# Performance work log

Hardware: AMD Instinct MI355X
Metric: run time of the kernel (lower is better)

The kernel has to match this reference:

```python
import jax, jax.numpy as jnp
import numpy as np

D = 33        # n_vertices
HID = 256     # hidden_features
N_RANKS = 5


def setup_inputs() -> dict:
    key = jax.random.key(0)
    ks = jax.random.split(key, 8)
    img = jax.random.uniform(ks[0], (1, 3, 2160, 3840), dtype=jnp.float32)
    param = jax.random.normal(ks[1], (1, N_RANKS), dtype=jnp.float32) * 0.1

    def lin(k, fan_in, fan_out):
        lim = 1.0 / np.sqrt(fan_in)
        kw, kb = jax.random.split(k)
        W = jax.random.uniform(kw, (fan_in, fan_out), minval=-lim, maxval=lim, dtype=jnp.float32)
        b = jax.random.uniform(kb, (fan_out,), minval=-lim, maxval=lim, dtype=jnp.float32)
        return W, b

    W0, b0 = lin(ks[2], 11, HID)
    W1, b1 = lin(ks[3], HID, HID)
    W2, b2 = lin(ks[4], HID, HID)
    W3, b3 = lin(ks[5], HID, HID)
    W4, b4 = lin(ks[6], HID, 3)
    return dict(img=img, param=param, W0=W0, b0=b0, W1=W1, b1=b1,
                W2=W2, b2=b2, W3=W3, b3=b3, W4=W4, b4=b4)


def _identity_lut_flat():
    # torch: stack(meshgrid(ij), 0)/ (D-1), flip(0), reshape (1,3,D^3)
    v = jnp.arange(D, dtype=jnp.float32)
    g = jnp.stack(jnp.meshgrid(v, v, v, indexing='ij'), axis=0) / (D - 1)
    return g[::-1].reshape(1, 3, -1)  # (1, 3, 35937)


def _nilut(intensity, W0, b0, W1, b1, W2, b2, W3, b3, W4, b4):
    # intensity: (B, N, 8) = [r, g, b, params...]
    inp = jnp.concatenate([intensity, jnp.sort(intensity[..., :3], axis=-1)], axis=-1)  # (B,N,11)
    zero_inp = inp[:1].at[:, :, 3:-3].set(0.0)  # zero the param channels

    def net(x):
        h = jax.nn.relu(x @ W0 + b0)
        h = jnp.tanh(h @ W1 + b1)
        h = jnp.tanh(h @ W2 + b2)
        h = jnp.tanh(h @ W3 + b3)
        return h @ W4 + b4

    return net(inp) - net(zero_inp) + intensity[..., :3]


def _trilinear_lookup(img, luts):
    # img: (B,3,H,W) in [0,1]; luts: (B,3,D,D,D) indexed [c, b_idx, g_idx, r_idx]
    s = img * (D - 1)
    idx = jnp.clip(jnp.floor(s), 0, D - 2).astype(jnp.int32)
    f = s - idx.astype(s.dtype)

    def one(lut_b, idx_b, f_b):
        ir, ig, ib = idx_b[0], idx_b[1], idx_b[2]
        fr, fg, fb = f_b[0], f_b[1], f_b[2]

        def g(db, dg, dr):
            return lut_b[:, ib + db, ig + dg, ir + dr]  # (3,H,W)

        return (g(0, 0, 0) * (1 - fb) * (1 - fg) * (1 - fr)
                + g(0, 0, 1) * (1 - fb) * (1 - fg) * fr
                + g(0, 1, 0) * (1 - fb) * fg * (1 - fr)
                + g(0, 1, 1) * (1 - fb) * fg * fr
                + g(1, 0, 0) * fb * (1 - fg) * (1 - fr)
                + g(1, 0, 1) * fb * (1 - fg) * fr
                + g(1, 1, 0) * fb * fg * (1 - fr)
                + g(1, 1, 1) * fb * fg * fr)

    return jax.vmap(one)(luts, idx, f)


def reference(img, param, W0, b0, W1, b1, W2, b2, W3, b3, W4, b4):
    B = param.shape[0]
    ident = _identity_lut_flat()                              # (1,3,N)
    Nl = ident.shape[2]
    tiled = jnp.broadcast_to(param[:, :, None], (B, N_RANKS, Nl))
    ins = jnp.concatenate([jnp.broadcast_to(ident, (B, 3, Nl)), tiled], axis=1)  # (B,8,N)
    ins = jnp.transpose(ins, (0, 2, 1))                       # (B,N,8)
    luts = _nilut(ins, W0, b0, W1, b1, W2, b2, W3, b3, W4, b4)  # (B,N,3)
    luts = jnp.transpose(luts, (0, 2, 1)).reshape(B, 3, D, D, D)
    img_rep = jnp.broadcast_to(img, (B,) + img.shape[1:])
    return _trilinear_lookup(img_rep, luts)
```

## Files before the change

kernel.cpp:

```cpp
#include <hip/hip_runtime.h>
#include <hip/hip_fp16.h>
#include <math.h>

#define NPTS 35937
#define HID 256
#define TPB 256

typedef __attribute__((ext_vector_type(8))) short short8;
typedef __attribute__((ext_vector_type(4))) float f32x4;

__device__ __forceinline__ float fast_tanh(float x) {
    float e = __expf(2.0f * x);
    return 1.0f - __fdividef(2.0f, e + 1.0f);
}

__device__ __forceinline__ short f2bf(float f) {
    union { float f; unsigned u; } v; v.f = f;
    unsigned r = (v.u + 0x7fffu + ((v.u >> 16) & 1u)) >> 16;
    return (short)r;
}

#define W1P_OFF 8192
#define W2P_OFF 73728
#define W3P_OFF 139264
#define W4P_OFF 204800
#define LUT_BYTE_OFF 417792
#define CELL_BYTE_OFF 992896

__global__ __launch_bounds__(256) void pack_weights_kernel(
    const float* __restrict__ W0, const float* __restrict__ W1,
    const float* __restrict__ W2, const float* __restrict__ W3,
    const float* __restrict__ W4, short* __restrict__ P)
{
    int id = blockIdx.x * 256 + threadIdx.x;
    if (id >= 26112) return;
    const float* W; int f, NT, KREAL, NROW; long pbase;
    if (id < 1024)       { W = W0; f = id;         NT = 16; KREAL = 11;  NROW = 256; pbase = 0; }
    else if (id < 9216)  { W = W1; f = id - 1024;  NT = 16; KREAL = 256; NROW = 256; pbase = W1P_OFF; }
    else if (id < 17408) { W = W2; f = id - 9216;  NT = 16; KREAL = 256; NROW = 256; pbase = W2P_OFF; }
    else if (id < 25600) { W = W3; f = id - 17408; NT = 16; KREAL = 256; NROW = 256; pbase = W3P_OFF; }
    else                 { W = W4; f = id - 25600; NT = 1;  KREAL = 256; NROW = 3;   pbase = W4P_OFF; }
    int lane = f & 63;
    int tile = f >> 6;
    int nt = tile % NT, kt = tile / NT;
    int n  = nt * 16 + (lane & 15);
    int k0 = kt * 32 + ((lane >> 4) & 3) * 8;
    short v[8];
    #pragma unroll
    for (int j = 0; j < 8; ++j) {
        int k = k0 + j;
        float x = (k < KREAL && n < NROW) ? W[k * NROW + n] : 0.0f;
        v[j] = f2bf(x);
    }
    *(short8*)(P + pbase + (long)f * 8) = *(short8*)v;
}

#define HSTR 264

__global__ __launch_bounds__(256) void nilut_mfma_kernel(
    const float* __restrict__ param, const short* __restrict__ P,
    const float* __restrict__ b0, const float* __restrict__ b1,
    const float* __restrict__ b2, const float* __restrict__ b3,
    const float* __restrict__ b4, float* __restrict__ lut4)
{
    __shared__ short Hs[64][HSTR];
    __shared__ short Is[64][40];
    __shared__ float OB[64][4];

    const int t = threadIdx.x;
    const int pblock = blockIdx.x * 32;
    const int lane = t & 63;
    const int wid  = t >> 6;
    const int lr = lane & 15;
    const int hi = lane >> 4;
    const int k8 = hi * 8;

    if (t < 64) {
        int pn = pblock + (t >> 1);
        if (pn >= NPTS) pn = NPTS - 1;
        int v = t & 1;
        int ii = pn / 1089;
        int rem = pn - ii * 1089;
        int jj = rem / 33;
        int kk = rem - jj * 33;
        float r = kk * (1.0f / 32.0f);
        float g = jj * (1.0f / 32.0f);
        float b = ii * (1.0f / 32.0f);
        float lo = fminf(r, fminf(g, b));
        float hv = fmaxf(r, fmaxf(g, b));
        float mid = r + g + b - lo - hv;
        Is[t][0] = f2bf(r); Is[t][1] = f2bf(g); Is[t][2] = f2bf(b);
        #pragma unroll
        for (int q = 0; q < 5; ++q)
            Is[t][3 + q] = (v == 0) ? f2bf(param[q]) : (short)0;
        Is[t][8] = f2bf(lo); Is[t][9] = f2bf(mid); Is[t][10] = f2bf(hv);
        #pragma unroll
        for (int q = 11; q < 40; ++q) Is[t][q] = (short)0;
    }
    __syncthreads();

    f32x4 acc[4][4];

    {
        #pragma unroll
        for (int c = 0; c < 4; ++c) {
            float bv = b0[wid * 64 + c * 16 + lr];
            f32x4 in = {bv, bv, bv, bv};
            #pragma unroll
            for (int rt = 0; rt < 4; ++rt) acc[rt][c] = in;
        }
        short8 a[4], bfr[4];
        #pragma unroll
        for (int rt = 0; rt < 4; ++rt) a[rt] = *(const short8*)&Is[rt * 16 + lr][k8];
        #pragma unroll
        for (int c = 0; c < 4; ++c)
            bfr[c] = *(const short8*)(P + ((long)(wid * 4 + c) * 64 + lane) * 8);
        #pragma unroll
        for (int rt = 0; rt < 4; ++rt)
            #pragma unroll
            for (int c = 0; c < 4; ++c)
                acc[rt][c] = __builtin_amdgcn_mfma_f32_16x16x32_bf16(a[rt], bfr[c], acc[rt][c], 0, 0, 0);
        #pragma unroll
        for (int rt = 0; rt < 4; ++rt)
            #pragma unroll
            for (int c = 0; c < 4; ++c)
                #pragma unroll
                for (int q = 0; q < 4; ++q)
                    Hs[rt * 16 + hi * 4 + q][wid * 64 + c * 16 + lr] = f2bf(fmaxf(acc[rt][c][q], 0.0f));
    }
    __syncthreads();

    const long loff[3] = {W1P_OFF, W2P_OFF, W3P_OFF};
    const float* bptr[3];
    bptr[0] = b1; bptr[1] = b2; bptr[2] = b3;
    for (int L = 0; L < 3; ++L) {
        const short* WL = P + loff[L];
        const float* bb = bptr[L];
        #pragma unroll
        for (int c = 0; c < 4; ++c) {
            float bv = bb[wid * 64 + c * 16 + lr];
            f32x4 in = {bv, bv, bv, bv};
            #pragma unroll
            for (int rt = 0; rt < 4; ++rt) acc[rt][c] = in;
        }
        #pragma unroll
        for (int kt = 0; kt < 8; ++kt) {
            short8 a[4], bfr[4];
            #pragma unroll
            for (int rt = 0; rt < 4; ++rt)
                a[rt] = *(const short8*)&Hs[rt * 16 + lr][kt * 32 + k8];
            #pragma unroll
            for (int c = 0; c < 4; ++c)
                bfr[c] = *(const short8*)(WL + ((long)(kt * 16 + wid * 4 + c) * 64 + lane) * 8);
            #pragma unroll
            for (int rt = 0; rt < 4; ++rt)
                #pragma unroll
                for (int c = 0; c < 4; ++c)
                    acc[rt][c] = __builtin_amdgcn_mfma_f32_16x16x32_bf16(a[rt], bfr[c], acc[rt][c], 0, 0, 0);
        }
        __syncthreads();
        #pragma unroll
        for (int rt = 0; rt < 4; ++rt)
            #pragma unroll
            for (int c = 0; c < 4; ++c)
                #pragma unroll
                for (int q = 0; q < 4; ++q)
                    Hs[rt * 16 + hi * 4 + q][wid * 64 + c * 16 + lr] = f2bf(fast_tanh(acc[rt][c][q]));
        __syncthreads();
    }

    {
        float bv = (lr < 3) ? b4[lr] : 0.0f;
        f32x4 a4 = {bv, bv, bv, bv};
        const short* WL = P + W4P_OFF;
        #pragma unroll
        for (int kt = 0; kt < 8; ++kt) {
            short8 a = *(const short8*)&Hs[wid * 16 + lr][kt * 32 + k8];
            short8 b = *(const short8*)(WL + ((long)kt * 64 + lane) * 8);
            a4 = __builtin_amdgcn_mfma_f32_16x16x32_bf16(a, b, a4, 0, 0, 0);
        }
        if (lr < 3) {
            #pragma unroll
            for (int q = 0; q < 4; ++q)
                OB[wid * 16 + hi * 4 + q][lr] = a4[q];
        }
    }
    __syncthreads();

    if (t < 96) {
        int pl = t / 3, c = t - pl * 3;
        int n = pblock + pl;
        if (n < NPTS) {
            int ii = n / 1089;
            int rem = n - ii * 1089;
            int jj = rem / 33;
            int kk = rem - jj * 33;
            float rgb = (c == 0) ? kk * (1.0f / 32.0f)
                      : (c == 1) ? jj * (1.0f / 32.0f)
                                 : ii * (1.0f / 32.0f);
            lut4[n * 4 + c] = OB[2 * pl][c] - OB[2 * pl + 1][c] + rgb;
        }
    }
}

__global__ __launch_bounds__(256) void expand_cells_kernel(
    const float* __restrict__ lut4, __half* __restrict__ cells)
{
    int id = blockIdx.x * 256 + threadIdx.x;
    if (id >= 32768 * 8) return;
    int corner = id & 7;
    int cell   = id >> 3;
    int ir = cell & 31, ig = (cell >> 5) & 31, ib = cell >> 10;
    int dr = corner & 1, dg = (corner >> 1) & 1, db = (corner >> 2) & 1;
    int src = (ib + db) * 1089 + (ig + dg) * 33 + (ir + dr);
    float4 v = *(const float4*)(lut4 + (long)src * 4);
    union { __half h[4]; uint2 u; } pk;
    pk.h[0] = __float2half_rn(v.x);
    pk.h[1] = __float2half_rn(v.y);
    pk.h[2] = __float2half_rn(v.z);
    pk.h[3] = __float2half_rn(0.0f);
    *(uint2*)(cells + (long)cell * 32 + corner * 4) = pk.u;
}

#define LERP(a, b, f) fmaf((f), (b) - (a), (a))

__global__ __launch_bounds__(256) void apply_lut_kernel(
    const float* __restrict__ img, const __half* __restrict__ cells,
    float* __restrict__ out)
{
    const int NP = 2160 * 3840;
    int idx = blockIdx.x * blockDim.x + threadIdx.x;
    int p = idx * 4;
    if (p >= NP) return;

    float4 rv = *(const float4*)(img + p);
    float4 gv = *(const float4*)(img + NP + p);
    float4 bv = *(const float4*)(img + 2 * NP + p);

    float rr[4] = {rv.x, rv.y, rv.z, rv.w};
    float gg[4] = {gv.x, gv.y, gv.z, gv.w};
    float bb[4] = {bv.x, bv.y, bv.z, bv.w};
    float ox[4], oy[4], oz[4];

    #pragma unroll
    for (int u = 0; u < 4; ++u) {
        float sr = rr[u] * 32.0f, sg = gg[u] * 32.0f, sb = bb[u] * 32.0f;
        float fir = fminf(fmaxf(floorf(sr), 0.0f), 31.0f);
        float fig = fminf(fmaxf(floorf(sg), 0.0f), 31.0f);
        float fib = fminf(fmaxf(floorf(sb), 0.0f), 31.0f);
        float fr = sr - fir, fg = sg - fig, fb = sb - fib;
        int ir = (int)fir, ig = (int)fig, ib = (int)fib;

        const short8* cb = (const short8*)(cells + ((long)(ib * 1024 + ig * 32 + ir)) * 32);
        union { short8 s; __half h[8]; } u0, u1, u2, u3;
        u0.s = cb[0];
        u1.s = cb[1];
        u2.s = cb[2];
        u3.s = cb[3];

        float v00[3], v01[3], v10[3], v11[3];
        #pragma unroll
        for (int c = 0; c < 3; ++c) {
            v00[c] = LERP(__half2float(u0.h[c]), __half2float(u0.h[c + 4]), fr);
            v01[c] = LERP(__half2float(u1.h[c]), __half2float(u1.h[c + 4]), fr);
            v10[c] = LERP(__half2float(u2.h[c]), __half2float(u2.h[c + 4]), fr);
            v11[c] = LERP(__half2float(u3.h[c]), __half2float(u3.h[c + 4]), fr);
        }
        ox[u] = LERP(LERP(v00[0], v01[0], fg), LERP(v10[0], v11[0], fg), fb);
        oy[u] = LERP(LERP(v00[1], v01[1], fg), LERP(v10[1], v11[1], fg), fb);
        oz[u] = LERP(LERP(v00[2], v01[2], fg), LERP(v10[2], v11[2], fg), fb);
    }

    *(float4*)(out + p)          = make_float4(ox[0], ox[1], ox[2], ox[3]);
    *(float4*)(out + NP + p)     = make_float4(oy[0], oy[1], oy[2], oy[3]);
    *(float4*)(out + 2 * NP + p) = make_float4(oz[0], oz[1], oz[2], oz[3]);
}

extern "C" void kernel_launch(void* const* d_in, const int* in_sizes, int n_in,
                              void* d_out, int out_size, void* d_ws, size_t ws_size,
                              hipStream_t stream) {
    const float* img   = (const float*)d_in[0];
    const float* param = (const float*)d_in[1];
    const float* W0 = (const float*)d_in[2];
    const float* b0 = (const float*)d_in[3];
    const float* W1 = (const float*)d_in[4];
    const float* b1 = (const float*)d_in[5];
    const float* W2 = (const float*)d_in[6];
    const float* b2 = (const float*)d_in[7];
    const float* W3 = (const float*)d_in[8];
    const float* b3 = (const float*)d_in[9];
    const float* W4 = (const float*)d_in[10];
    const float* b4 = (const float*)d_in[11];

    short*  P     = (short*)d_ws;
    float*  lut4  = (float*)((char*)d_ws + LUT_BYTE_OFF);
    __half* cells = (__half*)((char*)d_ws + CELL_BYTE_OFF);
    float*  out   = (float*)d_out;

    hipLaunchKernelGGL(pack_weights_kernel, dim3(102), dim3(TPB), 0, stream,
                       W0, W1, W2, W3, W4, P);

    int lut_blocks = (NPTS + 31) / 32;
    hipLaunchKernelGGL(nilut_mfma_kernel, dim3(lut_blocks), dim3(TPB), 0, stream,
                       param, P, b0, b1, b2, b3, b4, lut4);

    hipLaunchKernelGGL(expand_cells_kernel, dim3(1024), dim3(TPB), 0, stream,
                       lut4, cells);

    const int NP = 2160 * 3840;
    int apply_blocks = (NP / 4 + TPB - 1) / TPB;
    hipLaunchKernelGGL(apply_lut_kernel, dim3(apply_blocks), dim3(TPB), 0, stream,
                       img, cells, out);
}
```

Measured before the change: 142.3 us.

## Pack LUT cell corners into 11-11-10 bit quantized words with global range

Each LUT cell corner changes from four fp16 values (8 bytes) to one 32-bit word holding 11/11/10-bit unsigned codes. The codes are scaled by a global min/max found with atomics in the NILUT kernel. This halves the per-cell gather in the apply kernel from 64 to 32 bytes, cutting cache and memory traffic for the random LUT reads. In exchange it adds integer unpacking and an extra dequantize step, and it loses precision (about 1/1023 of the range for the third channel), which may break the accuracy tolerance.

```diff
diff --git a/kernel.cpp b/kernel.cpp
--- a/kernel.cpp
+++ b/kernel.cpp
@@ -1,6 +1,6 @@
 #include <hip/hip_runtime.h>
-#include <hip/hip_fp16.h>
 #include <math.h>
+#include <stdint.h>
 
 #define NPTS 35937
 #define HID 256
@@ -18,6 +18,15 @@
     union { float f; unsigned u; } v; v.f = f;
     unsigned r = (v.u + 0x7fffu + ((v.u >> 16) & 1u)) >> 16;
     return (short)r;
+}
+
+__device__ __forceinline__ unsigned f2ord(float f) {
+    unsigned u = __float_as_uint(f);
+    return (u & 0x80000000u) ? ~u : (u | 0x80000000u);
+}
+__device__ __forceinline__ float ord2f(unsigned o) {
+    unsigned u = (o & 0x80000000u) ? (o & 0x7fffffffu) : ~o;
+    return __uint_as_float(u);
 }
 
 #define W1P_OFF 8192
@@ -25,14 +34,17 @@
 #define W3P_OFF 139264
 #define W4P_OFF 204800
 #define LUT_BYTE_OFF 417792
-#define CELL_BYTE_OFF 992896
+#define RNG_BYTE_OFF 992784
+#define CELL_BYTE_OFF 1048576
 
 __global__ __launch_bounds__(256) void pack_weights_kernel(
     const float* __restrict__ W0, const float* __restrict__ W1,
     const float* __restrict__ W2, const float* __restrict__ W3,
-    const float* __restrict__ W4, short* __restrict__ P)
+    const float* __restrict__ W4, short* __restrict__ P,
+    unsigned* __restrict__ rng)
 {
     int id = blockIdx.x * 256 + threadIdx.x;
+    if (id == 0) { rng[0] = 0xFFFFFFFFu; rng[1] = 0u; }
     if (id >= 26112) return;
     const float* W; int f, NT, KREAL, NROW; long pbase;
     if (id < 1024)       { W = W0; f = id;         NT = 16; KREAL = 11;  NROW = 256; pbase = 0; }
@@ -61,7 +73,8 @@
     const float* __restrict__ param, const short* __restrict__ P,
     const float* __restrict__ b0, const float* __restrict__ b1,
     const float* __restrict__ b2, const float* __restrict__ b3,
-    const float* __restrict__ b4, float* __restrict__ lut4)
+    const float* __restrict__ b4, float* __restrict__ lut4,
+    unsigned* __restrict__ rng)
 {
     __shared__ short Hs[64][HSTR];
     __shared__ short Is[64][40];
@@ -187,6 +200,7 @@
     }
     __syncthreads();
 
+    float vmn = INFINITY, vmx = -INFINITY;
     if (t < 96) {
         int pl = t / 3, c = t - pl * 3;
         int n = pblock + pl;
@@ -198,13 +212,25 @@
             float rgb = (c == 0) ? kk * (1.0f / 32.0f)
                       : (c == 1) ? jj * (1.0f / 32.0f)
                                  : ii * (1.0f / 32.0f);
-            lut4[n * 4 + c] = OB[2 * pl][c] - OB[2 * pl + 1][c] + rgb;
-        }
+            float val = OB[2 * pl][c] - OB[2 * pl + 1][c] + rgb;
+            lut4[n * 4 + c] = val;
+            vmn = val; vmx = val;
+        }
+    }
+    #pragma unroll
+    for (int off = 32; off; off >>= 1) {
+        vmn = fminf(vmn, __shfl_xor(vmn, off));
+        vmx = fmaxf(vmx, __shfl_xor(vmx, off));
+    }
+    if (lane == 0 && vmn <= vmx) {
+        atomicMin(&rng[0], f2ord(vmn));
+        atomicMax(&rng[1], f2ord(vmx));
     }
 }
 
 __global__ __launch_bounds__(256) void expand_cells_kernel(
-    const float* __restrict__ lut4, __half* __restrict__ cells)
+    const float* __restrict__ lut4, const unsigned* __restrict__ rng,
+    unsigned* __restrict__ cells)
 {
     int id = blockIdx.x * 256 + threadIdx.x;
     if (id >= 32768 * 8) return;
@@ -214,24 +240,38 @@
     int dr = corner & 1, dg = (corner >> 1) & 1, db = (corner >> 2) & 1;
     int src = (ib + db) * 1089 + (ig + dg) * 33 + (ir + dr);
     float4 v = *(const float4*)(lut4 + (long)src * 4);
-    union { __half h[4]; uint2 u; } pk;
-    pk.h[0] = __float2half_rn(v.x);
-    pk.h[1] = __float2half_rn(v.y);
-    pk.h[2] = __float2half_rn(v.z);
-    pk.h[3] = __float2half_rn(0.0f);
-    *(uint2*)(cells + (long)cell * 32 + corner * 4) = pk.u;
+
+    float mn = ord2f(rng[0]);
+    float mx = ord2f(rng[1]);
+    float span = fmaxf(mx - mn, 1e-9f);
+    float i01 = 2047.0f / span;
+    float i2  = 1023.0f / span;
+
+    unsigned c0 = __float2uint_rn(fmaxf(v.x - mn, 0.0f) * i01); c0 = min(c0, 2047u);
+    unsigned c1 = __float2uint_rn(fmaxf(v.y - mn, 0.0f) * i01); c1 = min(c1, 2047u);
+    unsigned c2 = __float2uint_rn(fmaxf(v.z - mn, 0.0f) * i2);  c2 = min(c2, 1023u);
+    cells[(long)cell * 8 + corner] = c0 | (c1 << 11) | (c2 << 22);
 }
 
 #define LERP(a, b, f) fmaf((f), (b) - (a), (a))
+#define CH0(w) ((float)((w) & 2047u))
+#define CH1(w) ((float)(((w) >> 11) & 2047u))
+#define CH2(w) ((float)((w) >> 22))
 
 __global__ __launch_bounds__(256) void apply_lut_kernel(
-    const float* __restrict__ img, const __half* __restrict__ cells,
-    float* __restrict__ out)
+    const float* __restrict__ img, const unsigned* __restrict__ cells,
+    const unsigned* __restrict__ rng, float* __restrict__ out)
 {
     const int NP = 2160 * 3840;
     int idx = blockIdx.x * blockDim.x + threadIdx.x;
     int p = idx * 4;
     if (p >= NP) return;
+
+    float mn = ord2f(rng[0]);
+    float mx = ord2f(rng[1]);
+    float span = fmaxf(mx - mn, 1e-9f);
+    float st01 = span * (1.0f / 2047.0f);
+    float st2  = span * (1.0f / 1023.0f);
 
     float4 rv = *(const float4*)(img + p);
     float4 gv = *(const float4*)(img + NP + p);
@@ -251,24 +291,24 @@
         float fr = sr - fir, fg = sg - fig, fb = sb - fib;
         int ir = (int)fir, ig = (int)fig, ib = (int)fib;
 
-        const short8* cb = (const short8*)(cells + ((long)(ib * 1024 + ig * 32 + ir)) * 32);
-        union { short8 s; __half h[8]; } u0, u1, u2, u3;
-        u0.s = cb[0];
-        u1.s = cb[1];
-        u2.s = cb[2];
-        u3.s = cb[3];
-
-        float v00[3], v01[3], v10[3], v11[3];
-        #pragma unroll
-        for (int c = 0; c < 3; ++c) {
-            v00[c] = LERP(__half2float(u0.h[c]), __half2float(u0.h[c + 4]), fr);
-            v01[c] = LERP(__half2float(u1.h[c]), __half2float(u1.h[c + 4]), fr);
-            v10[c] = LERP(__half2float(u2.h[c]), __half2float(u2.h[c + 4]), fr);
-            v11[c] = LERP(__half2float(u3.h[c]), __half2float(u3.h[c + 4]), fr);
-        }
-        ox[u] = LERP(LERP(v00[0], v01[0], fg), LERP(v10[0], v11[0], fg), fb);
-        oy[u] = LERP(LERP(v00[1], v01[1], fg), LERP(v10[1], v11[1], fg), fb);
-        oz[u] = LERP(LERP(v00[2], v01[2], fg), LERP(v10[2], v11[2], fg), fb);
+        const uint4* C = ((const uint4*)cells) + (((size_t)(ib * 1024 + ig * 32 + ir)) << 1);
+        uint4 w0 = C[0];
+        uint4 w1 = C[1];
+
+        float x00 = LERP(CH0(w0.x), CH0(w0.y), fr), x01 = LERP(CH0(w0.z), CH0(w0.w), fr);
+        float x10 = LERP(CH0(w1.x), CH0(w1.y), fr), x11 = LERP(CH0(w1.z), CH0(w1.w), fr);
+        float xc  = LERP(LERP(x00, x01, fg), LERP(x10, x11, fg), fb);
+        ox[u] = fmaf(xc, st01, mn);
+
+        float y00 = LERP(CH1(w0.x), CH1(w0.y), fr), y01 = LERP(CH1(w0.z), CH1(w0.w), fr);
+        float y10 = LERP(CH1(w1.x), CH1(w1.y), fr), y11 = LERP(CH1(w1.z), CH1(w1.w), fr);
+        float yc  = LERP(LERP(y00, y01, fg), LERP(y10, y11, fg), fb);
+        oy[u] = fmaf(yc, st01, mn);
+
+        float z00 = LERP(CH2(w0.x), CH2(w0.y), fr), z01 = LERP(CH2(w0.z), CH2(w0.w), fr);
+        float z10 = LERP(CH2(w1.x), CH2(w1.y), fr), z11 = LERP(CH2(w1.z), CH2(w1.w), fr);
+        float zc  = LERP(LERP(z00, z01, fg), LERP(z10, z11, fg), fb);
+        oz[u] = fmaf(zc, st2, mn);
     }
 
     *(float4*)(out + p)          = make_float4(ox[0], ox[1], ox[2], ox[3]);
@@ -292,23 +332,24 @@
     const float* W4 = (const float*)d_in[10];
     const float* b4 = (const float*)d_in[11];
 
-    short*  P     = (short*)d_ws;
-    float*  lut4  = (float*)((char*)d_ws + LUT_BYTE_OFF);
-    __half* cells = (__half*)((char*)d_ws + CELL_BYTE_OFF);
-    float*  out   = (float*)d_out;
+    short*    P     = (short*)d_ws;
+    float*    lut4  = (float*)((char*)d_ws + LUT_BYTE_OFF);
+    unsigned* rng   = (unsigned*)((char*)d_ws + RNG_BYTE_OFF);
+    unsigned* cells = (unsigned*)((char*)d_ws + CELL_BYTE_OFF);
+    float*    out   = (float*)d_out;
 
     hipLaunchKernelGGL(pack_weights_kernel, dim3(102), dim3(TPB), 0, stream,
-                       W0, W1, W2, W3, W4, P);
+                       W0, W1, W2, W3, W4, P, rng);
 
     int lut_blocks = (NPTS + 31) / 32;
     hipLaunchKernelGGL(nilut_mfma_kernel, dim3(lut_blocks), dim3(TPB), 0, stream,
-                       param, P, b0, b1, b2, b3, b4, lut4);
+                       param, P, b0, b1, b2, b3, b4, lut4, rng);
 
     hipLaunchKernelGGL(expand_cells_kernel, dim3(1024), dim3(TPB), 0, stream,
-                       lut4, cells);
+                       lut4, rng, cells);
 
     const int NP = 2160 * 3840;
     int apply_blocks = (NP / 4 + TPB - 1) / TPB;
     hipLaunchKernelGGL(apply_lut_kernel, dim3(apply_blocks), dim3(TPB), 0, stream,
-                       img, cells, out);
-}
+                       img, cells, rng, out);
+}
```

New measurement: 165.7 us. +16.5%, slower.
